# Kernel tuning notes

Hardware: AMD Instinct MI355X
Metric: run time of the kernel (lower is better)

Reference implementation:

```python
import jax, jax.numpy as jnp
import numpy as np
import math

N = 20000          # nodes
E = 320000         # edges (avg degree 16)
NS, NV = 16, 4     # scalar / vector multiplicities
NCAT = 10
CAT_VOCAB = 119
DIST_DIM = 32
LIG_MAX_R = 5.0
W1_NUMEL = NS * NS + NS * NV          # 320 : layer1 tp weights
W2_NUMEL = NS * NS + NV * NS + NS * NV + NV * NV + NV * NV  # 416


def setup_inputs() -> dict:
    key = jax.random.key(0)
    ks = jax.random.split(key, 24)
    s = 0.1
    inp = {
        'x_cat': jax.random.randint(ks[0], (N, NCAT), 0, 2),
        'x_scalar': jax.random.normal(ks[1], (N, 32), jnp.float32),
        'pos': jax.random.normal(ks[2], (N, 3), jnp.float32) * 3.0,
        'edge_index': jax.random.randint(ks[3], (2, E), 0, N),
        'edge_bond': jax.random.uniform(ks[4], (E, 10), jnp.float32),
        # AtomEncoder params
        'emb_tables': jax.random.normal(ks[5], (NCAT, CAT_VOCAB, NS)) * s,
        'node_w': jax.random.normal(ks[6], (32, NS)) * s,
        'node_b': jnp.zeros((NS,), jnp.float32),
        # lig_edge_embedding MLP (42 -> ns -> ns)
        'em_w1': jax.random.normal(ks[7], (10 + DIST_DIM, NS)) * s,
        'em_b1': jnp.zeros((NS,), jnp.float32),
        'em_w2': jax.random.normal(ks[8], (NS, NS)) * s,
        'em_b2': jnp.zeros((NS,), jnp.float32),
        'c1_w1': jax.random.normal(ks[9], (3 * NS, 3 * NS)) * s,
        'c1_b1': jnp.zeros((3 * NS,), jnp.float32),
        'c1_w2': jax.random.normal(ks[10], (3 * NS, W1_NUMEL)) * s,
        'c1_b2': jnp.zeros((W1_NUMEL,), jnp.float32),
        # conv layer 2 fc
        'c2_w1': jax.random.normal(ks[11], (3 * NS, 3 * NS)) * s,
        'c2_b1': jnp.zeros((3 * NS,), jnp.float32),
        'c2_w2': jax.random.normal(ks[12], (3 * NS, W2_NUMEL)) * s,
        'c2_b2': jnp.zeros((W2_NUMEL,), jnp.float32),
    }
    return inp


def _scatter_mean(vals, idx, n):
    s = jax.ops.segment_sum(vals, idx, num_segments=n)
    cnt = jax.ops.segment_sum(jnp.ones(idx.shape, vals.dtype), idx, num_segments=n)
    return s / jnp.maximum(cnt, 1.0)[:, None]


def _forward(x_cat, x_scalar, pos, edge_index, edge_bond,
             emb_tables, node_w, node_b, em_w1, em_b1, em_w2, em_b2,
             c1_w1, c1_b1, c1_w2, c1_b2, c2_w1, c2_b1, c2_w2, c2_b2):
    ns, nv = NS, NV
    n = x_cat.shape[0]
    # ---- AtomEncoder: sum of categorical embeddings + linear(scalar) ----
    gathered = emb_tables[jnp.arange(NCAT)[None, :], x_cat]      # [N, 10, ns]
    node = gathered.sum(axis=1) + x_scalar @ node_w + node_b    # [N, ns]

    src, dst = edge_index[0], edge_index[1]
    vec = pos[dst] - pos[src]                                   # [E, 3]
    dist = jnp.sqrt(jnp.sum(vec * vec, axis=-1) + 1e-12)
    unit = vec / (dist + 1e-8)[:, None]
    # spherical harmonics, lmax=1, component normalization: [1, sqrt(3)*r_hat]
    sh0 = jnp.ones((vec.shape[0], 1), vec.dtype)
    sh1 = math.sqrt(3.0) * unit                                 # [E, 3]

    # ---- GaussianSmearing + edge embedding MLP ----
    offset = jnp.linspace(0.0, LIG_MAX_R, DIST_DIM)
    coeff = -0.5 / float(LIG_MAX_R / (DIST_DIM - 1)) ** 2
    demb = jnp.exp(coeff * (dist[:, None] - offset[None, :]) ** 2)
    e_in = jnp.concatenate([edge_bond, demb], axis=1)           # [E, 42]
    edge_emb = jax.nn.relu(e_in @ em_w1 + em_b1) @ em_w2 + em_b2  # [E, ns]

    # ======== conv layer 1: ns x0e -> ns x0e + nv x1o ========
    ea = jnp.concatenate([edge_emb, node[src, :ns], node[dst, :ns]], axis=1)
    w = jax.nn.relu(ea @ c1_w1 + c1_b1) @ c1_w2 + c1_b2         # [E, 320]
    wa = w[:, :ns * ns].reshape(-1, ns, ns)
    wb = w[:, ns * ns:].reshape(-1, ns, nv)
    s_dst = node[dst]                                           # [E, ns]
    a = 1.0 / math.sqrt(ns)                                     # fan-in norm
    out0 = jnp.einsum('euk,eu->ek', wa, s_dst) * sh0 * a        # 0e x 0e -> 0e
    out1 = jnp.einsum('euw,eu->ew', wb, s_dst)[:, :, None] * sh1[:, None, :] * a
    tp = jnp.concatenate([out0, out1.reshape(-1, 3 * nv)], axis=1)
    node = _scatter_mean(tp, src, n)                            # [N, ns+3nv]

    # ======== conv layer 2: ns x0e + nv x1o -> ns x0e + nv x1o + nv x1e ====
    ea = jnp.concatenate([edge_emb, node[src, :ns], node[dst, :ns]], axis=1)
    w = jax.nn.relu(ea @ c2_w1 + c2_b1) @ c2_w2 + c2_b2         # [E, 416]
    o = 0
    wa = w[:, o:o + ns * ns].reshape(-1, ns, ns); o += ns * ns
    wb = w[:, o:o + nv * ns].reshape(-1, nv, ns); o += nv * ns
    wc = w[:, o:o + ns * nv].reshape(-1, ns, nv); o += ns * nv
    wd = w[:, o:o + nv * nv].reshape(-1, nv, nv); o += nv * nv
    we = w[:, o:o + nv * nv].reshape(-1, nv, nv)
    s = node[dst, :ns]
    v = node[dst, ns:].reshape(-1, nv, 3)
    a0 = 1.0 / math.sqrt(ns + nv)   # two paths into 0e
    a1 = 1.0 / math.sqrt(ns + nv)   # two paths into 1o
    aE = 1.0 / math.sqrt(nv)        # one path into 1e
    vdot = jnp.einsum('evi,ei->ev', v, sh1)                     # 1o . 1o
    out0 = (jnp.einsum('euk,eu->ek', wa, s) * sh0
            + jnp.einsum('euk,eu->ek', wb, vdot) / math.sqrt(3.0)) * a0
    out1o = (jnp.einsum('euw,eu->ew', wc, s)[:, :, None] * sh1[:, None, :]
             + jnp.einsum('euw,eui->ewi', wd, v) * sh0[:, :, None]) * a1
    crossv = jnp.cross(v, jnp.broadcast_to(sh1[:, None, :], v.shape))
    out1e = jnp.einsum('euw,eui->ewi', we, crossv) * (aE / math.sqrt(2.0))
    tp = jnp.concatenate([out0, out1o.reshape(-1, 3 * nv),
                          out1e.reshape(-1, 3 * nv)], axis=1)
    node = _scatter_mean(tp, src, n)                            # [N, ns+6nv] = [N,40]
    return node


def reference(x_cat, x_scalar, pos, edge_index, edge_bond,
              emb_tables, node_w, node_b, em_w1, em_b1, em_w2, em_b2,
              c1_w1, c1_b1, c1_w2, c1_b2, c2_w1, c2_b1, c2_w2, c2_b2):
    return _forward(x_cat, x_scalar, pos, edge_index, edge_bond,
                    emb_tables, node_w, node_b, em_w1, em_b1, em_w2, em_b2,
                    c1_w1, c1_b1, c1_w2, c1_b2, c2_w1, c2_b1, c2_w2, c2_b2)
```

## Files before the change

### kernel.cpp

```cpp
#include <hip/hip_runtime.h>
#include <math.h>

#define NN 20000
#define NE 320000

typedef _Float16 f16x8 __attribute__((ext_vector_type(8)));
typedef float f32x4 __attribute__((ext_vector_type(4)));
typedef unsigned short ushort_t;
typedef unsigned int uint_t;

#define MFMA16(A,B,C) __builtin_amdgcn_mfma_f32_16x16x32_f16((A),(B),(C),0,0,0)
#define LDS_FENCE() do{ asm volatile("s_waitcnt lgkmcnt(0)" ::: "memory"); __builtin_amdgcn_sched_barrier(0);}while(0)

static_assert(NE % 256 == 0, "edge grid must tile exactly");

__device__ __forceinline__ float frelu(float x){ return fmaxf(x, 0.0f); }

__device__ __forceinline__ void splitf(float x, ushort_t& h, ushort_t& l){
    _Float16 hh = (_Float16)x;
    float r = (x - (float)hh) * 2048.0f;
    _Float16 ll = (_Float16)r;
    union { _Float16 f; ushort_t u; } ch, cl;
    ch.f = hh; cl.f = ll;
    h = ch.u; l = cl.u;
}

__device__ __forceinline__ void edge_embed(
    int e, int s, int d,
    const float* __restrict__ pos,
    const float* __restrict__ edge_bond,
    const float* __restrict__ em_w1, const float* __restrict__ em_b1,
    const float* __restrict__ em_w2, const float* __restrict__ em_b2,
    float* eemb, float* sh1)
{
    float vx = pos[d*3+0] - pos[s*3+0];
    float vy = pos[d*3+1] - pos[s*3+1];
    float vz = pos[d*3+2] - pos[s*3+2];
    float d2 = vx*vx + vy*vy + vz*vz + 1e-12f;
    float dist = sqrtf(d2);
    float inv = 1.0f / (dist + 1e-8f);
    const float SQ3 = 1.7320508075688772f;
    sh1[0] = SQ3 * vx * inv;
    sh1[1] = SQ3 * vy * inv;
    sh1[2] = SQ3 * vz * inv;

    float ein[42];
    #pragma unroll
    for (int t = 0; t < 10; ++t) ein[t] = edge_bond[e*10 + t];
    const float coeff = -19.22f;
    const float step  = 5.0f / 31.0f;
    #pragma unroll
    for (int k = 0; k < 32; ++k) {
        float dd = dist - step * (float)k;
        ein[10+k] = __expf(coeff * dd * dd);
    }

    float t1[16];
    #pragma unroll
    for (int j = 0; j < 16; ++j) t1[j] = em_b1[j];
    #pragma unroll
    for (int t = 0; t < 42; ++t) {
        float v = ein[t];
        #pragma unroll
        for (int j = 0; j < 16; ++j) t1[j] += v * em_w1[t*16 + j];
    }
    #pragma unroll
    for (int j = 0; j < 16; ++j) t1[j] = frelu(t1[j]);

    #pragma unroll
    for (int j = 0; j < 16; ++j) eemb[j] = em_b2[j];
    #pragma unroll
    for (int t = 0; t < 16; ++t) {
        float v = t1[t];
        #pragma unroll
        for (int j = 0; j < 16; ++j) eemb[j] += v * em_w2[t*16 + j];
    }
}

template<int STRIDE>
__device__ __forceinline__ void compute_h(
    int e, int s, int d,
    const float* __restrict__ pos, const float* __restrict__ edge_bond,
    const float* __restrict__ em_w1, const float* __restrict__ em_b1,
    const float* __restrict__ em_w2, const float* __restrict__ em_b2,
    const float* __restrict__ w1, const float* __restrict__ b1,
    const float* __restrict__ node, float* h, float* sh1, float* sdout)
{
    float ea[48];
    edge_embed(e, s, d, pos, edge_bond, em_w1, em_b1, em_w2, em_b2, ea, sh1);
    const float4* rs = reinterpret_cast<const float4*>(node + (size_t)s*STRIDE);
    const float4* rd = reinterpret_cast<const float4*>(node + (size_t)d*STRIDE);
    #pragma unroll
    for (int k = 0; k < 4; ++k) {
        float4 q = rs[k];
        ea[16+4*k] = q.x; ea[17+4*k] = q.y; ea[18+4*k] = q.z; ea[19+4*k] = q.w;
        float4 r = rd[k];
        ea[32+4*k] = r.x; ea[33+4*k] = r.y; ea[34+4*k] = r.z; ea[35+4*k] = r.w;
    }
    #pragma unroll
    for (int k = 0; k < 16; ++k) sdout[k] = ea[32+k];
    #pragma unroll
    for (int j = 0; j < 48; ++j) h[j] = b1[j];
    #pragma unroll
    for (int t = 0; t < 48; ++t) {
        float v = ea[t];
        #pragma unroll
        for (int j = 0; j < 48; ++j) h[j] += v * w1[t*48 + j];
    }
    #pragma unroll
    for (int j = 0; j < 48; ++j) h[j] = frelu(h[j]);
}

template<int NC>
__device__ __forceinline__ void stage_B(ushort_t* sB,
                                        const float* __restrict__ w2,
                                        const float* __restrict__ b2,
                                        int t0, int ntl, int tid)
{
    int nslots = ntl << 7;
    for (int slot = tid; slot < nslots; slot += 256) {
        int tl = slot >> 7; int r7 = slot & 127; int kb = r7 >> 6; int ll = r7 & 63;
        int col = (t0 + tl)*16 + (ll & 15);
        int k0 = (kb<<5) + ((ll>>4)<<3);
        uint_t hw[4], lw[4];
        #pragma unroll
        for (int p = 0; p < 4; ++p) {
            int ka = k0 + 2*p, kb2 = k0 + 2*p + 1;
            float va = (ka < 48) ? w2[ka*NC + col] : (ka == 48 ? b2[col] : 0.0f);
            float vb = (kb2 < 48) ? w2[kb2*NC + col] : (kb2 == 48 ? b2[col] : 0.0f);
            ushort_t ah, al, bh, bl;
            splitf(va, ah, al);
            splitf(vb, bh, bl);
            hw[p] = (uint_t)ah | ((uint_t)bh << 16);
            lw[p] = (uint_t)al | ((uint_t)bl << 16);
        }
        int base = tl*2048 + kb*1024 + ll*8;
        *reinterpret_cast<uint4*>(&sB[base])       = make_uint4(hw[0], hw[1], hw[2], hw[3]);
        *reinterpret_cast<uint4*>(&sB[base + 512]) = make_uint4(lw[0], lw[1], lw[2], lw[3]);
    }
}

__device__ __forceinline__ void stage_A(ushort_t* bounce, int l,
                                        const uint_t* hph, const uint_t* hpl,
                                        f16x8 ahi[4][2], f16x8 alo[4][2])
{
    *reinterpret_cast<uint4*>(&bounce[l*16])     = make_uint4(0,0,0,0);
    *reinterpret_cast<uint4*>(&bounce[l*16 + 8]) = make_uint4(0,0,0,0);
    LDS_FENCE();
    #pragma unroll
    for (int mt = 0; mt < 4; ++mt) {
        bool act = ((l >> 4) == mt);
        if (act) {
            #pragma unroll
            for (int jj = 0; jj < 25; ++jj) {
                int k = jj*2, kb = k >> 5, kk = k & 31;
                int lr = (l & 15) + ((kk >> 3) << 4);
                *reinterpret_cast<uint_t*>(&bounce[kb*512 + lr*8 + (kk & 7)]) = hph[jj];
            }
        }
        LDS_FENCE();
        ahi[mt][0] = *reinterpret_cast<const f16x8*>(&bounce[l*8]);
        ahi[mt][1] = *reinterpret_cast<const f16x8*>(&bounce[512 + l*8]);
        LDS_FENCE();
        if (act) {
            #pragma unroll
            for (int jj = 0; jj < 25; ++jj) {
                int k = jj*2, kb = k >> 5, kk = k & 31;
                int lr = (l & 15) + ((kk >> 3) << 4);
                *reinterpret_cast<uint_t*>(&bounce[kb*512 + lr*8 + (kk & 7)]) = hpl[jj];
            }
        }
        LDS_FENCE();
        alo[mt][0] = *reinterpret_cast<const f16x8*>(&bounce[l*8]);
        alo[mt][1] = *reinterpret_cast<const f16x8*>(&bounce[512 + l*8]);
        LDS_FENCE();
    }
}

__global__ __launch_bounds__(256)
void k_node_feat(const int* __restrict__ x_cat, const float* __restrict__ x_scalar,
                 const float* __restrict__ emb, const float* __restrict__ node_w,
                 const float* __restrict__ node_b, float* __restrict__ node0)
{
    int n = blockIdx.x * 256 + threadIdx.x;
    if (n >= NN) return;
    float acc[16];
    #pragma unroll
    for (int k = 0; k < 16; ++k) acc[k] = node_b[k];
    #pragma unroll
    for (int c = 0; c < 10; ++c) {
        int idx = x_cat[n*10 + c];
        const float4* row = reinterpret_cast<const float4*>(emb + (c*119 + idx)*16);
        #pragma unroll
        for (int k = 0; k < 4; ++k) {
            float4 q = row[k];
            acc[4*k+0] += q.x; acc[4*k+1] += q.y; acc[4*k+2] += q.z; acc[4*k+3] += q.w;
        }
    }
    #pragma unroll
    for (int t = 0; t < 32; ++t) {
        float xs = x_scalar[n*32 + t];
        #pragma unroll
        for (int k = 0; k < 16; ++k) acc[k] += xs * node_w[t*16 + k];
    }
    #pragma unroll
    for (int k = 0; k < 16; ++k) node0[n*16 + k] = acc[k];
}

__global__ __launch_bounds__(256)
void k_edge_l1(const int* __restrict__ ei, const float* __restrict__ pos,
               const float* __restrict__ edge_bond,
               const float* __restrict__ em_w1, const float* __restrict__ em_b1,
               const float* __restrict__ em_w2, const float* __restrict__ em_b2,
               const float* __restrict__ w1, const float* __restrict__ b1,
               const float* __restrict__ w2, const float* __restrict__ b2,
               const float* __restrict__ node0,
               float* __restrict__ accum, float* __restrict__ cnt)
{
    __shared__ __align__(16) ushort_t sB[7*2048];
    __shared__ __align__(16) float    sT[16*260];
    __shared__ float sSh[256*3];
    __shared__ int   sSrc[256];

    int tid = threadIdx.x;
    int l = tid & 63;
    int cc = l & 15;
    int e = blockIdx.x*256 + tid;
    int s = ei[e], d = ei[NE + e];

    float h[48], sh1[3], sd[16];
    compute_h<16>(e, s, d, pos, edge_bond, em_w1, em_b1, em_w2, em_b2, w1, b1,
                  node0, h, sh1, sd);
    atomicAdd(cnt + s, 1.0f);
    sSrc[tid] = s;
    #pragma unroll
    for (int u = 0; u < 16; ++u) sT[u*260 + tid] = sd[u];
    #pragma unroll
    for (int k = 0; k < 3; ++k) sSh[tid*3 + k] = sh1[k];

    uint_t hph[25], hpl[25];
    #pragma unroll
    for (int jj = 0; jj < 24; ++jj) {
        ushort_t ah, al, bh, bl;
        splitf(h[2*jj],   ah, al);
        splitf(h[2*jj+1], bh, bl);
        hph[jj] = (uint_t)ah | ((uint_t)bh << 16);
        hpl[jj] = (uint_t)al | ((uint_t)bl << 16);
    }
    hph[24] = 0x3C00u;
    hpl[24] = 0u;

    f16x8 ahi[4][2], alo[4][2];
    stage_A(sB + (tid >> 6)*1024, l, hph, hpl, ahi, alo);

    f32x4 out0[4];
    float ob[4][4];
    #pragma unroll
    for (int mt = 0; mt < 4; ++mt) {
        out0[mt] = (f32x4){0.f,0.f,0.f,0.f};
        #pragma unroll
        for (int r = 0; r < 4; ++r) ob[mt][r] = 0.f;
    }

    for (int c0 = 0; c0 < 20; c0 += 7) {
        int ntl = (20 - c0 < 7) ? (20 - c0) : 7;
        __syncthreads();
        stage_B<320>(sB, w2, b2, c0, ntl, tid);
        __syncthreads();
        for (int tl = 0; tl < ntl; ++tl) {
            int t = c0 + tl;
            int bb = tl*2048 + l*8;
            f16x8 bh0 = *reinterpret_cast<const f16x8*>(&sB[bb]);
            f16x8 bl0 = *reinterpret_cast<const f16x8*>(&sB[bb + 512]);
            f16x8 bh1 = *reinterpret_cast<const f16x8*>(&sB[bb + 1024]);
            f16x8 bl1 = *reinterpret_cast<const f16x8*>(&sB[bb + 1536]);
            #pragma unroll
            for (int mt = 0; mt < 4; ++mt) {
                f32x4 Dh = (f32x4){0.f,0.f,0.f,0.f};
                f32x4 Dc = (f32x4){0.f,0.f,0.f,0.f};
                Dh = MFMA16(ahi[mt][0], bh0, Dh);
                Dh = MFMA16(ahi[mt][1], bh1, Dh);
                Dc = MFMA16(alo[mt][0], bh0, Dc);
                Dc = MFMA16(ahi[mt][0], bl0, Dc);
                Dc = MFMA16(alo[mt][1], bh1, Dc);
                Dc = MFMA16(ahi[mt][1], bl1, Dc);
                f32x4 D = Dh + Dc * 0.00048828125f;
                int elb = (tid & 192) + (mt << 4) + ((l >> 4) << 2);
                if (t < 16) {
                    f32x4 sv = *reinterpret_cast<const f32x4*>(&sT[t*260 + elb]);
                    out0[mt] += sv * D;
                } else {
                    const float* sp = &sT[(((t-16)<<2) + (cc>>2))*260 + elb];
                    #pragma unroll
                    for (int r = 0; r < 4; ++r) ob[mt][r] += sp[r] * D[r];
                }
            }
        }
    }

    #pragma unroll
    for (int mt = 0; mt < 4; ++mt) {
        int elb = (tid & 192) + (mt << 4) + ((l >> 4) << 2);
        #pragma unroll
        for (int r = 0; r < 4; ++r) {
            int el = elb + r;
            int sidx = sSrc[el];
            atomicAdd(accum + (size_t)sidx*28 + cc, out0[mt][r] * 0.25f);
            float x = ob[mt][r];
            x += __shfl_xor(x, 4); x += __shfl_xor(x, 8);
            int q = cc / 3; int i = cc - q*3;
            float xq = __shfl(x, (l & 48) | q);
            if (cc < 12)
                atomicAdd(accum + (size_t)sidx*28 + 16 + cc, 0.25f * xq * sSh[el*3 + i]);
        }
    }
}

__global__ __launch_bounds__(256)
void k_edge_l2(const int* __restrict__ ei, const float* __restrict__ pos,
               const float* __restrict__ edge_bond,
               const float* __restrict__ em_w1, const float* __restrict__ em_b1,
               const float* __restrict__ em_w2, const float* __restrict__ em_b2,
               const float* __restrict__ w1, const float* __restrict__ b1,
               const float* __restrict__ w2, const float* __restrict__ b2,
               const float* __restrict__ node1,
               float* __restrict__ accum2)
{
    __shared__ __align__(16) ushort_t sB[8*2048];
    __shared__ __align__(16) float    sT[16*260];
    __shared__ __align__(16) float    sVd[4*260];
    __shared__ float sSh[256*3];
    __shared__ int   sSrc[256];
    __shared__ int   sDst[256];

    int tid = threadIdx.x;
    int l = tid & 63;
    int cc = l & 15;
    int e = blockIdx.x*256 + tid;
    int s = ei[e], d = ei[NE + e];

    float h[48], sh1[3], sd[16];
    compute_h<28>(e, s, d, pos, edge_bond, em_w1, em_b1, em_w2, em_b2, w1, b1,
                  node1, h, sh1, sd);
    sSrc[tid] = s;
    sDst[tid] = d;
    #pragma unroll
    for (int u = 0; u < 16; ++u) sT[u*260 + tid] = sd[u];
    #pragma unroll
    for (int k = 0; k < 3; ++k) sSh[tid*3 + k] = sh1[k];
    {
        const float4* rv = reinterpret_cast<const float4*>(node1 + (size_t)d*28 + 16);
        float4 a = rv[0], b = rv[1], c = rv[2];
        float vv[12] = {a.x,a.y,a.z,a.w, b.x,b.y,b.z,b.w, c.x,c.y,c.z,c.w};
        const float INV_SQ3 = 0.5773502691896258f;
        #pragma unroll
        for (int u = 0; u < 4; ++u)
            sVd[u*260 + tid] = (vv[u*3]*sh1[0] + vv[u*3+1]*sh1[1] + vv[u*3+2]*sh1[2]) * INV_SQ3;
    }

    uint_t hph[25], hpl[25];
    #pragma unroll
    for (int jj = 0; jj < 24; ++jj) {
        ushort_t ah, al, bh, bl;
        splitf(h[2*jj],   ah, al);
        splitf(h[2*jj+1], bh, bl);
        hph[jj] = (uint_t)ah | ((uint_t)bh << 16);
        hpl[jj] = (uint_t)al | ((uint_t)bl << 16);
    }
    hph[24] = 0x3C00u;
    hpl[24] = 0u;

    f16x8 ahi[4][2], alo[4][2];
    stage_A(sB + (tid >> 6)*1024, l, hph, hpl, ahi, alo);

    const float A0 = 0.22360679774997896f;
    const float AE = 0.3535533905932738f;

    f32x4 out0[4];
    float outc[4][4];
    #pragma unroll
    for (int mt = 0; mt < 4; ++mt) {
        out0[mt] = (f32x4){0.f,0.f,0.f,0.f};
        #pragma unroll
        for (int r = 0; r < 4; ++r) outc[mt][r] = 0.f;
    }

    for (int c0 = 0; c0 < 26; c0 += 8) {
        int ntl = (26 - c0 < 8) ? (26 - c0) : 8;
        __syncthreads();
        stage_B<416>(sB, w2, b2, c0, ntl, tid);
        __syncthreads();
        for (int tl = 0; tl < ntl; ++tl) {
            int t = c0 + tl;
            int bb = tl*2048 + l*8;
            f16x8 bh0 = *reinterpret_cast<const f16x8*>(&sB[bb]);
            f16x8 bl0 = *reinterpret_cast<const f16x8*>(&sB[bb + 512]);
            f16x8 bh1 = *reinterpret_cast<const f16x8*>(&sB[bb + 1024]);
            f16x8 bl1 = *reinterpret_cast<const f16x8*>(&sB[bb + 1536]);
            #pragma unroll
            for (int mt = 0; mt < 4; ++mt) {
                f32x4 Dh = (f32x4){0.f,0.f,0.f,0.f};
                f32x4 Dc = (f32x4){0.f,0.f,0.f,0.f};
                Dh = MFMA16(ahi[mt][0], bh0, Dh);
                Dh = MFMA16(ahi[mt][1], bh1, Dh);
                Dc = MFMA16(alo[mt][0], bh0, Dc);
                Dc = MFMA16(ahi[mt][0], bl0, Dc);
                Dc = MFMA16(alo[mt][1], bh1, Dc);
                Dc = MFMA16(ahi[mt][1], bl1, Dc);
                f32x4 D = Dh + Dc * 0.00048828125f;
                int elb = (tid & 192) + (mt << 4) + ((l >> 4) << 2);
                if (t < 16) {
                    f32x4 sv = *reinterpret_cast<const f32x4*>(&sT[t*260 + elb]);
                    out0[mt] += sv * D;
                } else if (t < 20) {
                    f32x4 vd = *reinterpret_cast<const f32x4*>(&sVd[(t-16)*260 + elb]);
                    out0[mt] += vd * D;
                } else if (t < 24) {
                    const float* sp = &sT[(((t-20)<<2) + (cc>>2))*260 + elb];
                    #pragma unroll
                    for (int r = 0; r < 4; ++r) outc[mt][r] += sp[r] * D[r];
                } else if (t == 24) {
                    #pragma unroll
                    for (int r = 0; r < 4; ++r) {
                        int el = elb + r;
                        int dv = sDst[el];
                        const float* vp = node1 + (size_t)dv*28 + 16 + (cc>>2)*3;
                        float a0 = D[r]*vp[0], a1 = D[r]*vp[1], a2 = D[r]*vp[2];
                        a0 += __shfl_xor(a0,4); a0 += __shfl_xor(a0,8);
                        a1 += __shfl_xor(a1,4); a1 += __shfl_xor(a1,8);
                        a2 += __shfl_xor(a2,4); a2 += __shfl_xor(a2,8);
                        float xc = outc[mt][r];
                        xc += __shfl_xor(xc,4); xc += __shfl_xor(xc,8);
                        int q = cc / 3; int i = cc - q*3;
                        int srcl = (l & 48) | q;
                        float g0 = __shfl(a0, srcl), g1 = __shfl(a1, srcl), g2 = __shfl(a2, srcl);
                        float oo = (i==0) ? g0 : ((i==1) ? g1 : g2);
                        float xq = __shfl(xc, srcl);
                        if (cc < 12) {
                            float sh1i = sSh[el*3 + i];
                            atomicAdd(accum2 + (size_t)sSrc[el]*40 + 16 + cc,
                                      A0 * (xq * sh1i + oo));
                        }
                    }
                } else {
                    #pragma unroll
                    for (int r = 0; r < 4; ++r) {
                        int el = elb + r;
                        int dv = sDst[el];
                        const float* vp = node1 + (size_t)dv*28 + 16 + (cc>>2)*3;
                        float vx = vp[0], vy = vp[1], vz = vp[2];
                        float sx = sSh[el*3+0], sy = sSh[el*3+1], sz = sSh[el*3+2];
                        float cx = vy*sz - vz*sy;
                        float cy = vz*sx - vx*sz;
                        float cz = vx*sy - vy*sx;
                        float a0 = D[r]*cx, a1 = D[r]*cy, a2 = D[r]*cz;
                        a0 += __shfl_xor(a0,4); a0 += __shfl_xor(a0,8);
                        a1 += __shfl_xor(a1,4); a1 += __shfl_xor(a1,8);
                        a2 += __shfl_xor(a2,4); a2 += __shfl_xor(a2,8);
                        int q = cc / 3; int i = cc - q*3;
                        int srcl = (l & 48) | q;
                        float g0 = __shfl(a0, srcl), g1 = __shfl(a1, srcl), g2 = __shfl(a2, srcl);
                        float oo = (i==0) ? g0 : ((i==1) ? g1 : g2);
                        if (cc < 12)
                            atomicAdd(accum2 + (size_t)sSrc[el]*40 + 28 + cc, AE * oo);
                    }
                }
            }
        }
    }

    #pragma unroll
    for (int mt = 0; mt < 4; ++mt) {
        int elb = (tid & 192) + (mt << 4) + ((l >> 4) << 2);
        #pragma unroll
        for (int r = 0; r < 4; ++r) {
            int el = elb + r;
            atomicAdd(accum2 + (size_t)sSrc[el]*40 + cc, out0[mt][r] * A0);
        }
    }
}

__global__ __launch_bounds__(256)
void k_div(const float* in, float* out, const float* __restrict__ cnt, int cols, int total)
{
    int i = blockIdx.x * 256 + threadIdx.x;
    if (i >= total) return;
    int n = i / cols;
    out[i] = in[i] / fmaxf(cnt[n], 1.0f);
}

extern "C" void kernel_launch(void* const* d_in, const int* in_sizes, int n_in,
                              void* d_out, int out_size, void* d_ws, size_t ws_size,
                              hipStream_t stream) {
    const int*   x_cat     = (const int*)  d_in[0];
    const float* x_scalar  = (const float*)d_in[1];
    const float* pos       = (const float*)d_in[2];
    const int*   ei        = (const int*)  d_in[3];
    const float* edge_bond = (const float*)d_in[4];
    const float* emb       = (const float*)d_in[5];
    const float* node_w    = (const float*)d_in[6];
    const float* node_b    = (const float*)d_in[7];
    const float* em_w1     = (const float*)d_in[8];
    const float* em_b1     = (const float*)d_in[9];
    const float* em_w2     = (const float*)d_in[10];
    const float* em_b2     = (const float*)d_in[11];
    const float* c1_w1     = (const float*)d_in[12];
    const float* c1_b1     = (const float*)d_in[13];
    const float* c1_w2     = (const float*)d_in[14];
    const float* c1_b2     = (const float*)d_in[15];
    const float* c2_w1     = (const float*)d_in[16];
    const float* c2_b1     = (const float*)d_in[17];
    const float* c2_w2     = (const float*)d_in[18];
    const float* c2_b2     = (const float*)d_in[19];

    float* ws     = (float*)d_ws;
    float* node0  = ws;
    float* accum1 = ws + 320000;
    float* accum2 = ws + 880000;
    float* cnt    = ws + 1680000;

    hipMemsetAsync(accum1, 0, (size_t)(560000 + 800000 + 20000) * sizeof(float), stream);

    k_node_feat<<<(NN + 255) / 256, 256, 0, stream>>>(
        x_cat, x_scalar, emb, node_w, node_b, node0);

    k_edge_l1<<<NE / 256, 256, 0, stream>>>(
        ei, pos, edge_bond, em_w1, em_b1, em_w2, em_b2,
        c1_w1, c1_b1, c1_w2, c1_b2, node0, accum1, cnt);

    k_div<<<(560000 + 255) / 256, 256, 0, stream>>>(accum1, accum1, cnt, 28, 560000);

    k_edge_l2<<<NE / 256, 256, 0, stream>>>(
        ei, pos, edge_bond, em_w1, em_b1, em_w2, em_b2,
        c2_w1, c2_b1, c2_w2, c2_b2, accum1, accum2);

    k_div<<<(800000 + 255) / 256, 256, 0, stream>>>(accum2, (float*)d_out, cnt, 40, 800000);
}
```

Measured before the change: 341.5 us.

## Prepack fp16 hi/lo weight tiles once in a separate kernel, copy into LDS

Adds a small kernel that converts the second-layer fc weights and bias into the split fp16 hi/lo MFMA tile layout once per call. Each edge block now copies prepacked tiles from global memory into LDS instead of reading strided fp32 and splitting per block. The A-operand staging writes hi and lo halves in a single pass with fewer LDS fences, using a larger bounce buffer per wave. Layer 2 chunk size drops from 8 to 6 tiles to fit LDS, which adds more chunk iterations and barriers.

Result: no change. 340.6 us (-0.2%).

```diff
diff --git a/kernel.cpp b/kernel.cpp
--- a/kernel.cpp
+++ b/kernel.cpp
@@ -111,68 +111,65 @@
     for (int j = 0; j < 48; ++j) h[j] = frelu(h[j]);
 }
 
-template<int NC>
-__device__ __forceinline__ void stage_B(ushort_t* sB,
-                                        const float* __restrict__ w2,
-                                        const float* __restrict__ b2,
-                                        int t0, int ntl, int tid)
-{
-    int nslots = ntl << 7;
-    for (int slot = tid; slot < nslots; slot += 256) {
-        int tl = slot >> 7; int r7 = slot & 127; int kb = r7 >> 6; int ll = r7 & 63;
-        int col = (t0 + tl)*16 + (ll & 15);
-        int k0 = (kb<<5) + ((ll>>4)<<3);
-        uint_t hw[4], lw[4];
-        #pragma unroll
-        for (int p = 0; p < 4; ++p) {
-            int ka = k0 + 2*p, kb2 = k0 + 2*p + 1;
-            float va = (ka < 48) ? w2[ka*NC + col] : (ka == 48 ? b2[col] : 0.0f);
-            float vb = (kb2 < 48) ? w2[kb2*NC + col] : (kb2 == 48 ? b2[col] : 0.0f);
-            ushort_t ah, al, bh, bl;
-            splitf(va, ah, al);
-            splitf(vb, bh, bl);
-            hw[p] = (uint_t)ah | ((uint_t)bh << 16);
-            lw[p] = (uint_t)al | ((uint_t)bl << 16);
-        }
-        int base = tl*2048 + kb*1024 + ll*8;
-        *reinterpret_cast<uint4*>(&sB[base])       = make_uint4(hw[0], hw[1], hw[2], hw[3]);
-        *reinterpret_cast<uint4*>(&sB[base + 512]) = make_uint4(lw[0], lw[1], lw[2], lw[3]);
-    }
+__global__ __launch_bounds__(256)
+void k_pack(const float* __restrict__ w2, const float* __restrict__ b2,
+            ushort_t* __restrict__ out, int NC, int ntiles)
+{
+    int slot = blockIdx.x*256 + threadIdx.x;
+    if (slot >= ntiles*128) return;
+    int tl = slot >> 7; int r7 = slot & 127; int kb = r7 >> 6; int ll = r7 & 63;
+    int col = tl*16 + (ll & 15);
+    int k0 = (kb<<5) + ((ll>>4)<<3);
+    uint_t hw[4], lw[4];
+    #pragma unroll
+    for (int p = 0; p < 4; ++p) {
+        int ka = k0 + 2*p, kb2 = k0 + 2*p + 1;
+        float va = (ka < 48) ? w2[ka*NC + col] : (ka == 48 ? b2[col] : 0.0f);
+        float vb = (kb2 < 48) ? w2[kb2*NC + col] : (kb2 == 48 ? b2[col] : 0.0f);
+        ushort_t ah, al, bh, bl;
+        splitf(va, ah, al);
+        splitf(vb, bh, bl);
+        hw[p] = (uint_t)ah | ((uint_t)bh << 16);
+        lw[p] = (uint_t)al | ((uint_t)bl << 16);
+    }
+    int base = tl*2048 + kb*1024 + ll*8;
+    *reinterpret_cast<uint4*>(&out[base])       = make_uint4(hw[0], hw[1], hw[2], hw[3]);
+    *reinterpret_cast<uint4*>(&out[base + 512]) = make_uint4(lw[0], lw[1], lw[2], lw[3]);
+}
+
+__device__ __forceinline__ void copy_chunk(ushort_t* sB, const ushort_t* __restrict__ g,
+                                           int c0, int ntl, int tid)
+{
+    const uint4* gp = reinterpret_cast<const uint4*>(g) + c0*256;
+    uint4* sp = reinterpret_cast<uint4*>(sB);
+    for (int i = tid; i < ntl*256; i += 256) sp[i] = gp[i];
 }
 
 __device__ __forceinline__ void stage_A(ushort_t* bounce, int l,
                                         const uint_t* hph, const uint_t* hpl,
                                         f16x8 ahi[4][2], f16x8 alo[4][2])
 {
-    *reinterpret_cast<uint4*>(&bounce[l*16])     = make_uint4(0,0,0,0);
-    *reinterpret_cast<uint4*>(&bounce[l*16 + 8]) = make_uint4(0,0,0,0);
+    #pragma unroll
+    for (int t = 0; t < 4; ++t)
+        *reinterpret_cast<uint4*>(&bounce[l*32 + t*8]) = make_uint4(0,0,0,0);
     LDS_FENCE();
     #pragma unroll
     for (int mt = 0; mt < 4; ++mt) {
-        bool act = ((l >> 4) == mt);
-        if (act) {
+        if ((l >> 4) == mt) {
             #pragma unroll
             for (int jj = 0; jj < 25; ++jj) {
                 int k = jj*2, kb = k >> 5, kk = k & 31;
                 int lr = (l & 15) + ((kk >> 3) << 4);
-                *reinterpret_cast<uint_t*>(&bounce[kb*512 + lr*8 + (kk & 7)]) = hph[jj];
+                int off = kb*512 + lr*8 + (kk & 7);
+                *reinterpret_cast<uint_t*>(&bounce[off])        = hph[jj];
+                *reinterpret_cast<uint_t*>(&bounce[1024 + off]) = hpl[jj];
             }
         }
         LDS_FENCE();
         ahi[mt][0] = *reinterpret_cast<const f16x8*>(&bounce[l*8]);
         ahi[mt][1] = *reinterpret_cast<const f16x8*>(&bounce[512 + l*8]);
-        LDS_FENCE();
-        if (act) {
-            #pragma unroll
-            for (int jj = 0; jj < 25; ++jj) {
-                int k = jj*2, kb = k >> 5, kk = k & 31;
-                int lr = (l & 15) + ((kk >> 3) << 4);
-                *reinterpret_cast<uint_t*>(&bounce[kb*512 + lr*8 + (kk & 7)]) = hpl[jj];
-            }
-        }
-        LDS_FENCE();
-        alo[mt][0] = *reinterpret_cast<const f16x8*>(&bounce[l*8]);
-        alo[mt][1] = *reinterpret_cast<const f16x8*>(&bounce[512 + l*8]);
+        alo[mt][0] = *reinterpret_cast<const f16x8*>(&bounce[1024 + l*8]);
+        alo[mt][1] = *reinterpret_cast<const f16x8*>(&bounce[1536 + l*8]);
         LDS_FENCE();
     }
 }
@@ -213,7 +210,7 @@
                const float* __restrict__ em_w1, const float* __restrict__ em_b1,
                const float* __restrict__ em_w2, const float* __restrict__ em_b2,
                const float* __restrict__ w1, const float* __restrict__ b1,
-               const float* __restrict__ w2, const float* __restrict__ b2,
+               const ushort_t* __restrict__ packW,
                const float* __restrict__ node0,
                float* __restrict__ accum, float* __restrict__ cnt)
 {
@@ -251,7 +248,7 @@
     hpl[24] = 0u;
 
     f16x8 ahi[4][2], alo[4][2];
-    stage_A(sB + (tid >> 6)*1024, l, hph, hpl, ahi, alo);
+    stage_A(sB + (tid >> 6)*2048, l, hph, hpl, ahi, alo);
 
     f32x4 out0[4];
     float ob[4][4];
@@ -265,7 +262,7 @@
     for (int c0 = 0; c0 < 20; c0 += 7) {
         int ntl = (20 - c0 < 7) ? (20 - c0) : 7;
         __syncthreads();
-        stage_B<320>(sB, w2, b2, c0, ntl, tid);
+        copy_chunk(sB, packW, c0, ntl, tid);
         __syncthreads();
         for (int tl = 0; tl < ntl; ++tl) {
             int t = c0 + tl;
@@ -322,11 +319,11 @@
                const float* __restrict__ em_w1, const float* __restrict__ em_b1,
                const float* __restrict__ em_w2, const float* __restrict__ em_b2,
                const float* __restrict__ w1, const float* __restrict__ b1,
-               const float* __restrict__ w2, const float* __restrict__ b2,
+               const ushort_t* __restrict__ packW,
                const float* __restrict__ node1,
                float* __restrict__ accum2)
 {
-    __shared__ __align__(16) ushort_t sB[8*2048];
+    __shared__ __align__(16) ushort_t sB[6*2048];
     __shared__ __align__(16) float    sT[16*260];
     __shared__ __align__(16) float    sVd[4*260];
     __shared__ float sSh[256*3];
@@ -371,7 +368,7 @@
     hpl[24] = 0u;
 
     f16x8 ahi[4][2], alo[4][2];
-    stage_A(sB + (tid >> 6)*1024, l, hph, hpl, ahi, alo);
+    stage_A(sB + (tid >> 6)*2048, l, hph, hpl, ahi, alo);
 
     const float A0 = 0.22360679774997896f;
     const float AE = 0.3535533905932738f;
@@ -385,10 +382,10 @@
         for (int r = 0; r < 4; ++r) outc[mt][r] = 0.f;
     }
 
-    for (int c0 = 0; c0 < 26; c0 += 8) {
-        int ntl = (26 - c0 < 8) ? (26 - c0) : 8;
+    for (int c0 = 0; c0 < 26; c0 += 6) {
+        int ntl = (26 - c0 < 6) ? (26 - c0) : 6;
         __syncthreads();
-        stage_B<416>(sB, w2, b2, c0, ntl, tid);
+        copy_chunk(sB, packW, c0, ntl, tid);
         __syncthreads();
         for (int tl = 0; tl < ntl; ++tl) {
             int t = c0 + tl;
@@ -518,21 +515,26 @@
     float* accum1 = ws + 320000;
     float* accum2 = ws + 880000;
     float* cnt    = ws + 1680000;
+    ushort_t* packA = (ushort_t*)(ws + 1700000);
+    ushort_t* packB = packA + 20*2048;
 
     hipMemsetAsync(accum1, 0, (size_t)(560000 + 800000 + 20000) * sizeof(float), stream);
+
+    k_pack<<<(20*128 + 255) / 256, 256, 0, stream>>>(c1_w2, c1_b2, packA, 320, 20);
+    k_pack<<<(26*128 + 255) / 256, 256, 0, stream>>>(c2_w2, c2_b2, packB, 416, 26);
 
     k_node_feat<<<(NN + 255) / 256, 256, 0, stream>>>(
         x_cat, x_scalar, emb, node_w, node_b, node0);
 
     k_edge_l1<<<NE / 256, 256, 0, stream>>>(
         ei, pos, edge_bond, em_w1, em_b1, em_w2, em_b2,
-        c1_w1, c1_b1, c1_w2, c1_b2, node0, accum1, cnt);
+        c1_w1, c1_b1, packA, node0, accum1, cnt);
 
     k_div<<<(560000 + 255) / 256, 256, 0, stream>>>(accum1, accum1, cnt, 28, 560000);
 
     k_edge_l2<<<NE / 256, 256, 0, stream>>>(
         ei, pos, edge_bond, em_w1, em_b1, em_w2, em_b2,
-        c2_w1, c2_b1, c2_w2, c2_b2, accum1, accum2);
+        c2_w1, c2_b1, packB, accum1, accum2);
 
     k_div<<<(800000 + 255) / 256, 256, 0, stream>>>(accum2, (float*)d_out, cnt, 40, 800000);
 }
```
